# Performance work log

Measured on AMD Instinct MI355X. Metric: run time of the kernel, lower is better.

Reference implementation:

```python
import jax, jax.numpy as jnp
import numpy as np

N_NODES = 8192
IN_F = 16384
OUT_F = 10
N_EDGES = 262144


def setup_inputs() -> dict:
    key = jax.random.key(0)
    ks = jax.random.split(key, 12)
    s = 0.02
    return {
        "x": jax.random.normal(ks[0], (N_NODES, IN_F), dtype=jnp.float32),
        "edge_index": jax.random.randint(ks[1], (2, N_EDGES), 0, N_NODES, dtype=jnp.int64),
        # lin1: in -> 4096, lin2: 4096 -> 2048 (torch Linear: y = x W^T + b)
        "lin1_w": jax.random.normal(ks[2], (4096, IN_F), dtype=jnp.float32) * s,
        "lin1_b": jnp.zeros((4096,), dtype=jnp.float32),
        "lin2_w": jax.random.normal(ks[3], (2048, 4096), dtype=jnp.float32) * s,
        "lin2_b": jnp.zeros((2048,), dtype=jnp.float32),
        # SAGEConv 1: 2048 -> 1024. lin_l (neighbor agg, with bias), lin_r (root, no bias)
        "s1_l_w": jax.random.normal(ks[4], (1024, 2048), dtype=jnp.float32) * s,
        "s1_l_b": jnp.zeros((1024,), dtype=jnp.float32),
        "s1_r_w": jax.random.normal(ks[5], (1024, 2048), dtype=jnp.float32) * s,
        # SAGEConv 2: 1024 -> OUT_F
        "s2_l_w": jax.random.normal(ks[6], (OUT_F, 1024), dtype=jnp.float32) * s,
        "s2_l_b": jnp.zeros((OUT_F,), dtype=jnp.float32),
        "s2_r_w": jax.random.normal(ks[7], (OUT_F, 1024), dtype=jnp.float32) * s,
    }


def reference(x, edge_index, lin1_w, lin1_b, lin2_w, lin2_b,
              s1_l_w, s1_l_b, s1_r_w, s2_l_w, s2_l_b, s2_r_w):
    n = x.shape[0]
    src, dst = edge_index[0], edge_index[1]
    # in-degree for mean aggregation; isolated nodes -> 0 aggregate (PyG behavior)
    deg = jax.ops.segment_sum(jnp.ones_like(dst, dtype=x.dtype), dst, num_segments=n)
    inv_deg = jnp.where(deg > 0, 1.0 / jnp.maximum(deg, 1.0), 0.0)[:, None]

    def sage(h, lw, lb, rw):
        # mean over incoming neighbor messages h[src] scattered to dst
        agg = jax.ops.segment_sum(h[src], dst, num_segments=n) * inv_deg
        return agg @ lw.T + lb + h @ rw.T

    h = jax.nn.relu(x @ lin1_w.T + lin1_b)
    h = jax.nn.relu(h @ lin2_w.T + lin2_b)
    # dropout layers act as identity in eval mode
    h = jax.nn.relu(sage(h, s1_l_w, s1_l_b, s1_r_w))
    h = jax.nn.relu(sage(h, s2_l_w, s2_l_b, s2_r_w))
    return jax.nn.softmax(h, axis=1)
```

## Files before the change

kernel.cpp:

```cpp
#include <hip/hip_runtime.h>


typedef short  short8   __attribute__((ext_vector_type(8)));
typedef float  floatx4  __attribute__((ext_vector_type(4)));
typedef unsigned short ushort8v __attribute__((ext_vector_type(8)));
typedef unsigned short ushort4v __attribute__((ext_vector_type(4)));
typedef unsigned short ushort;

__device__ __forceinline__ ushort f2bf(float f) {
  unsigned u = __float_as_uint(f);
  u += 0x7fffu + ((u >> 16) & 1u);
  return (ushort)(u >> 16);
}
__device__ __forceinline__ float bf2f(ushort h) {
  return __uint_as_float(((unsigned)h) << 16);
}

__device__ __forceinline__ void gload16(const void* g, void* l) {
  __builtin_amdgcn_global_load_lds(
      (const __attribute__((address_space(1))) void*)g,
      (__attribute__((address_space(3))) void*)l, 16, 0, 0);
}

__global__ __launch_bounds__(256) void cvt_f32_bf16(
    const float* __restrict__ in, ushort* __restrict__ out, long n8) {
  long i = (long)blockIdx.x * blockDim.x + threadIdx.x;
  const long stride = (long)gridDim.x * blockDim.x;
  for (; i < n8; i += stride) {
    const float4* p = (const float4*)(in + i * 8);
    float4 a = p[0], b = p[1];
    ushort8v o;
    o[0] = f2bf(a.x); o[1] = f2bf(a.y); o[2] = f2bf(a.z); o[3] = f2bf(a.w);
    o[4] = f2bf(b.x); o[5] = f2bf(b.y); o[6] = f2bf(b.z); o[7] = f2bf(b.w);
    *(ushort8v*)(out + i * 8) = o;
  }
}

__global__ void edge_count(const int* __restrict__ dst, int E, int* __restrict__ deg) {
  int e = blockIdx.x * 256 + threadIdx.x;
  if (e < E) atomicAdd(&deg[dst[e]], 1);
}

__global__ __launch_bounds__(256) void scan_k(
    const int* __restrict__ deg, int* __restrict__ offs, float* __restrict__ inv, int n) {
  __shared__ int part[256];
  const int t = threadIdx.x;
  int local[32];
  int s = 0;
  const int base = t * 32;
#pragma unroll
  for (int i = 0; i < 32; ++i) { local[i] = s; s += deg[base + i]; }
  part[t] = s;
  __syncthreads();
  for (int off = 1; off < 256; off <<= 1) {
    int v = (t >= off) ? part[t - off] : 0;
    __syncthreads();
    part[t] += v;
    __syncthreads();
  }
  const int prev = (t == 0) ? 0 : part[t - 1];
  if (t == 255) offs[n] = part[255];
#pragma unroll
  for (int i = 0; i < 32; ++i) {
    const int e = base + i;
    offs[e] = prev + local[i];
    const int d = deg[e];
    inv[e] = (d > 0) ? (1.0f / (float)d) : 0.0f;
  }
}

__global__ void edge_fill(const int* __restrict__ src, const int* __restrict__ dst, int E,
                          const int* __restrict__ offs, int* __restrict__ fill,
                          int* __restrict__ csr) {
  int e = blockIdx.x * 256 + threadIdx.x;
  if (e < E) {
    const int d = dst[e];
    const int p = offs[d] + atomicAdd(&fill[d], 1);
    csr[p] = src[e];
  }
}

template <int OUT_BF16, int RELU, int HAS_BIAS>
__global__ __launch_bounds__(512, 2) void gemm256(
    const ushort* __restrict__ A, const ushort* __restrict__ Bm,
    const float* __restrict__ bias, void* __restrict__ Cout,
    int M, int N, int K) {
  extern __shared__ char smem[];

  const int nbn = N >> 8;
  const int nbm8 = (M >> 8) >> 3;
  const int x = blockIdx.x & 7;
  const int j = blockIdx.x >> 3;
  const int bm = x * nbm8 + j / nbn;
  const int bn = j % nbn;

  const int t = threadIdx.x;
  const int w = t >> 6, lane = t & 63;
  const int wr = w >> 2, wc = w & 3;

  const int cswz = (t & 7) ^ ((t >> 3) & 7);
  const ushort* Ag = A  + (size_t)(bm * 256 + (t >> 3)) * K + cswz * 8;
  const ushort* Bg = Bm + (size_t)(bn * 256 + (t >> 3)) * K + cswz * 8;
  const int stOff = w * 1024;

  const int rA = wr * 128 + (lane & 15);
  const int rB = wc * 64 + (lane & 15);
  const int s0 = (((lane >> 4) ^ (lane & 7)) << 4);

  floatx4 acc[8][4] = {};
  const int NT = K >> 6;
  const int NIT = NT >> 1;

#define STGA(BUF, KT, H)                                                      \
  {                                                                           \
    const int k0_ = (((KT) < NT) ? (KT) : 0) << 6;                            \
    char* la_ = smem + (BUF) * 65536 + stOff;                                 \
    gload16(Ag + (size_t)(((H) * 2) * 64) * K + k0_, la_ + ((H) * 2) * 8192); \
    gload16(Ag + (size_t)(((H) * 2 + 1) * 64) * K + k0_,                      \
            la_ + ((H) * 2 + 1) * 8192);                                      \
  }
#define STGB(BUF, KT, H)                                                      \
  {                                                                           \
    const int k0_ = (((KT) < NT) ? (KT) : 0) << 6;                            \
    char* lb_ = smem + (BUF) * 65536 + 32768 + stOff;                         \
    gload16(Bg + (size_t)(((H) * 2) * 64) * K + k0_, lb_ + ((H) * 2) * 8192); \
    gload16(Bg + (size_t)(((H) * 2 + 1) * 64) * K + k0_,                      \
            lb_ + ((H) * 2 + 1) * 8192);                                      \
  }

#define PH(BUF, Q, READB, DOWAIT, ...)                                        \
  {                                                                           \
    const char* pa_ = smem + (BUF) * 65536 + rA * 128;                        \
    short8 a00 = *(const short8*)(pa_ + (2 * (Q)) * 2048 + s0);               \
    short8 a01 = *(const short8*)(pa_ + (2 * (Q)) * 2048 + (s0 ^ 64));        \
    short8 a10 = *(const short8*)(pa_ + (2 * (Q) + 1) * 2048 + s0);           \
    short8 a11 = *(const short8*)(pa_ + (2 * (Q) + 1) * 2048 + (s0 ^ 64));    \
    if (READB) {                                                              \
      const char* pb_ = smem + (BUF) * 65536 + 32768 + rB * 128;              \
      _Pragma("unroll") for (int ni = 0; ni < 4; ++ni) {                      \
        bfv0[ni] = *(const short8*)(pb_ + ni * 2048 + s0);                    \
        bfv1[ni] = *(const short8*)(pb_ + ni * 2048 + (s0 ^ 64));             \
      }                                                                       \
    }                                                                         \
    __VA_ARGS__;                                                              \
    if (DOWAIT) asm volatile("s_waitcnt vmcnt(4)" ::: "memory");              \
    __builtin_amdgcn_s_barrier();                                             \
    __builtin_amdgcn_s_setprio(1);                                            \
    _Pragma("unroll") for (int ni = 0; ni < 4; ++ni) {                        \
      acc[2 * (Q)][ni] = __builtin_amdgcn_mfma_f32_16x16x32_bf16(             \
          a00, bfv0[ni], acc[2 * (Q)][ni], 0, 0, 0);                          \
      acc[2 * (Q) + 1][ni] = __builtin_amdgcn_mfma_f32_16x16x32_bf16(         \
          a10, bfv0[ni], acc[2 * (Q) + 1][ni], 0, 0, 0);                      \
    }                                                                         \
    _Pragma("unroll") for (int ni = 0; ni < 4; ++ni) {                        \
      acc[2 * (Q)][ni] = __builtin_amdgcn_mfma_f32_16x16x32_bf16(             \
          a01, bfv1[ni], acc[2 * (Q)][ni], 0, 0, 0);                          \
      acc[2 * (Q) + 1][ni] = __builtin_amdgcn_mfma_f32_16x16x32_bf16(         \
          a11, bfv1[ni], acc[2 * (Q) + 1][ni], 0, 0, 0);                      \
    }                                                                         \
    __builtin_amdgcn_s_setprio(0);                                            \
    asm volatile("" ::: "memory");                                            \
  }

  STGA(0, 0, 0); STGA(0, 0, 1);
  STGB(0, 0, 0); STGB(0, 0, 1);
  STGB(1, 1, 0); STGB(1, 1, 1);
  asm volatile("s_waitcnt vmcnt(4)" ::: "memory");
  __builtin_amdgcn_s_barrier();
  asm volatile("" ::: "memory");

  for (int it = 0; it < NIT; ++it) {
    const int t1 = 2 * it + 1, t2 = 2 * it + 2, t3 = 2 * it + 3;
    short8 bfv0[4], bfv1[4];
    PH(0, 0, 1, 0, STGA(1, t1, 0); STGA(1, t1, 1));
    PH(0, 1, 0, 0, STGB(0, t2, 0));
    PH(0, 2, 0, 0, STGB(0, t2, 1));
    PH(0, 3, 0, 1, );
    PH(1, 0, 1, 0, STGA(0, t2, 0));
    PH(1, 1, 0, 0, STGA(0, t2, 1));
    PH(1, 2, 0, 0, STGB(1, t3, 0));
    PH(1, 3, 0, 1, STGB(1, t3, 1));
  }
  asm volatile("s_waitcnt vmcnt(0)" ::: "memory");

#undef STGA
#undef STGB
#undef PH

  const int row0 = bm * 256 + wr * 128 + ((lane >> 4) << 2);
  const int col0 = bn * 256 + wc * 64 + (lane & 15);
#pragma unroll
  for (int ni = 0; ni < 4; ++ni) {
    const int col = col0 + ni * 16;
    const float bv = HAS_BIAS ? bias[col] : 0.0f;
#pragma unroll
    for (int mi = 0; mi < 8; ++mi) {
#pragma unroll
      for (int j2 = 0; j2 < 4; ++j2) {
        const int row = row0 + mi * 16 + j2;
        float v = acc[mi][ni][j2] + bv;
        if (RELU) v = fmaxf(v, 0.0f);
        if (OUT_BF16)
          ((ushort*)Cout)[(size_t)row * N + col] = f2bf(v);
        else
          ((float*)Cout)[(size_t)row * N + col] = v;
      }
    }
  }
}

__global__ __launch_bounds__(256) void sage1_agg(
    const ushort* __restrict__ hlr1, const int* __restrict__ offs,
    const int* __restrict__ csr, const float* __restrict__ inv,
    const float* __restrict__ lb, ushort* __restrict__ h3) {
  const int dn = blockIdx.x;
  const int f4 = threadIdx.x * 4;
  float ax = 0.f, ay = 0.f, az = 0.f, aw = 0.f;
  const int e0 = offs[dn], e1 = offs[dn + 1];
  for (int e = e0; e < e1; ++e) {
    const int s = csr[e];
    const ushort4v v = *(const ushort4v*)(hlr1 + (size_t)s * 2048 + f4);
    ax += bf2f(v[0]); ay += bf2f(v[1]); az += bf2f(v[2]); aw += bf2f(v[3]);
  }
  const float iv = inv[dn];
  const ushort4v hr = *(const ushort4v*)(hlr1 + (size_t)dn * 2048 + 1024 + f4);
  const float4 bb = *(const float4*)(lb + f4);
  ushort4v o;
  o[0] = f2bf(fmaxf(ax * iv + bb.x + bf2f(hr[0]), 0.0f));
  o[1] = f2bf(fmaxf(ay * iv + bb.y + bf2f(hr[1]), 0.0f));
  o[2] = f2bf(fmaxf(az * iv + bb.z + bf2f(hr[2]), 0.0f));
  o[3] = f2bf(fmaxf(aw * iv + bb.w + bf2f(hr[3]), 0.0f));
  *(ushort4v*)(h3 + (size_t)dn * 1024 + f4) = o;
}

__global__ __launch_bounds__(256) void sage2_mm(
    const ushort* __restrict__ h3, const float* __restrict__ wl,
    const float* __restrict__ wr, float* __restrict__ hl2, float* __restrict__ hr2) {
  __shared__ float wds[20480];
  const int t = threadIdx.x;
  for (int i = t; i < 2560; i += 256)
    *(float4*)&wds[i * 4] = *(const float4*)&wl[i * 4];
  for (int i = t; i < 2560; i += 256)
    *(float4*)&wds[10240 + i * 4] = *(const float4*)&wr[i * 4];
  __syncthreads();

  const int r = t >> 4, c = t & 15;
  const int row = blockIdx.x * 16 + r;

  float hv[64];
#pragma unroll
  for (int ii = 0; ii < 8; ++ii) {
    ushort8v p = *(const ushort8v*)(h3 + (size_t)row * 1024 + c * 64 + ii * 8);
#pragma unroll
    for (int k = 0; k < 8; ++k) hv[ii * 8 + k] = bf2f(p[k]);
  }

  float al[10] = {}, ar[10] = {};
#pragma unroll
  for (int j = 0; j < 10; ++j) {
    const int base = j * 1024 + c * 64;
#pragma unroll
    for (int ii = 0; ii < 16; ++ii) {
      const int f = (ii + c) & 15;
      const float4 lv = *(const float4*)&wds[base + f * 4];
      const float4 rv = *(const float4*)&wds[10240 + base + f * 4];
      const float h0 = hv[f * 4], h1 = hv[f * 4 + 1],
                  h2 = hv[f * 4 + 2], h3v = hv[f * 4 + 3];
      al[j] = fmaf(h0, lv.x, fmaf(h1, lv.y, fmaf(h2, lv.z, fmaf(h3v, lv.w, al[j]))));
      ar[j] = fmaf(h0, rv.x, fmaf(h1, rv.y, fmaf(h2, rv.z, fmaf(h3v, rv.w, ar[j]))));
    }
  }
#pragma unroll
  for (int j = 0; j < 10; ++j) {
#pragma unroll
    for (int off = 8; off > 0; off >>= 1) {
      al[j] += __shfl_down(al[j], off);
      ar[j] += __shfl_down(ar[j], off);
    }
  }
  if (c == 0) {
#pragma unroll
    for (int j = 0; j < 10; ++j) {
      hl2[(size_t)row * 10 + j] = al[j];
      hr2[(size_t)row * 10 + j] = ar[j];
    }
  }
}

__global__ __launch_bounds__(64) void sage2_final(
    const float* __restrict__ hl2, const float* __restrict__ hr2,
    const int* __restrict__ offs, const int* __restrict__ csr,
    const float* __restrict__ inv, const float* __restrict__ lb,
    float* __restrict__ out) {
  const int dn = blockIdx.x;
  const int l = threadIdx.x;
  float a[10] = {};
  const int e0 = offs[dn], e1 = offs[dn + 1];
  for (int e = e0 + l; e < e1; e += 64) {
    const int s = csr[e];
#pragma unroll
    for (int j = 0; j < 10; ++j) a[j] += hl2[(size_t)s * 10 + j];
  }
#pragma unroll
  for (int j = 0; j < 10; ++j)
#pragma unroll
    for (int off = 32; off > 0; off >>= 1) a[j] += __shfl_down(a[j], off);
  if (l == 0) {
    const float iv = inv[dn];
    float v[10];
    float m = -1e30f;
#pragma unroll
    for (int j = 0; j < 10; ++j) {
      v[j] = fmaxf(a[j] * iv + lb[j] + hr2[(size_t)dn * 10 + j], 0.0f);
      m = fmaxf(m, v[j]);
    }
    float ssum = 0.0f;
#pragma unroll
    for (int j = 0; j < 10; ++j) { v[j] = __expf(v[j] - m); ssum += v[j]; }
    const float r = 1.0f / ssum;
#pragma unroll
    for (int j = 0; j < 10; ++j) out[(size_t)dn * 10 + j] = v[j] * r;
  }
}

extern "C" void kernel_launch(void* const* d_in, const int* in_sizes, int n_in,
                              void* d_out, int out_size, void* d_ws, size_t ws_size,
                              hipStream_t stream) {
  const float* x    = (const float*)d_in[0];
  const int*   ei   = (const int*)d_in[1];
  const float* w1   = (const float*)d_in[2];
  const float* b1   = (const float*)d_in[3];
  const float* w2   = (const float*)d_in[4];
  const float* b2   = (const float*)d_in[5];
  const float* s1lw = (const float*)d_in[6];
  const float* s1lb = (const float*)d_in[7];
  const float* s1rw = (const float*)d_in[8];
  const float* s2lw = (const float*)d_in[9];
  const float* s2lb = (const float*)d_in[10];
  const float* s2rw = (const float*)d_in[11];
  float* out = (float*)d_out;
  char* ws = (char*)d_ws;

  const int E = in_sizes[1] / 2;
  const int Nn = 8192;

  hipFuncSetAttribute((const void*)&gemm256<1, 1, 1>,
                      hipFuncAttributeMaxDynamicSharedMemorySize, 131072);
  hipFuncSetAttribute((const void*)&gemm256<1, 0, 0>,
                      hipFuncAttributeMaxDynamicSharedMemorySize, 131072);

  ushort* xb  = (ushort*)(ws + 0L);
  ushort* w1b = (ushort*)(ws + 268435456L);
  ushort* h1  = (ushort*)(ws + 402653184L);
  ushort* w2b = (ushort*)(ws + 469762048L);
  ushort* h2  = (ushort*)(ws + 486539264L);
  ushort* ws1 = (ushort*)(ws + 520093696L);
  char* csrb = ws + 528482304L;
  int*   deg  = (int*)(csrb);
  int*   fill = (int*)(csrb + 32768);
  int*   offs = (int*)(csrb + 65536);
  float* inv  = (float*)(csrb + 98816);
  int*   csr  = (int*)(csrb + 131584);
  ushort* hlr1 = (ushort*)(ws + 0L);
  ushort* h3   = (ushort*)(ws + 67108864L);
  float*  hl2  = (float*)(ws + 83886080L);
  float*  hr2  = (float*)(ws + 84213760L);

  const int* esrc = ei;
  const int* edst = ei + E;

  hipMemsetAsync(deg, 0, 65536, stream);

  cvt_f32_bf16<<<4096, 256, 0, stream>>>(x, xb, 16777216L);
  cvt_f32_bf16<<<2048, 256, 0, stream>>>(w1, w1b, 8388608L);
  cvt_f32_bf16<<<1024, 256, 0, stream>>>(w2, w2b, 1048576L);
  cvt_f32_bf16<<<256, 256, 0, stream>>>(s1lw, ws1, 262144L);
  cvt_f32_bf16<<<256, 256, 0, stream>>>(s1rw, ws1 + 2097152L, 262144L);

  edge_count<<<(E + 255) / 256, 256, 0, stream>>>(edst, E, deg);
  scan_k<<<1, 256, 0, stream>>>(deg, offs, inv, Nn);
  edge_fill<<<(E + 255) / 256, 256, 0, stream>>>(esrc, edst, E, offs, fill, csr);

  gemm256<1, 1, 1><<<512, 512, 131072, stream>>>(xb, w1b, b1, h1, 8192, 4096, 16384);
  gemm256<1, 1, 1><<<256, 512, 131072, stream>>>(h1, w2b, b2, h2, 8192, 2048, 4096);
  gemm256<1, 0, 0><<<256, 512, 131072, stream>>>(h2, ws1, nullptr, hlr1, 8192, 2048, 2048);

  sage1_agg<<<8192, 256, 0, stream>>>(hlr1, offs, csr, inv, s1lb, h3);
  sage2_mm<<<512, 256, 0, stream>>>(h3, s2lw, s2rw, hl2, hr2);
  sage2_final<<<8192, 64, 0, stream>>>(hl2, hr2, offs, csr, inv, s2lb, out);
}
```

Before: 1.365 ms.

## Fuse conversion launches, remap GEMM block swizzle, pack sage2_final nodes per block

Five separate fp32-to-bf16 conversion launches are merged into one grid-stride kernel to cut launch overhead and tail idle time. The GEMM block-index mapping now splits the N dimension, rather than M, across the 8-way XCD grouping, which changes which tiles share L2 on each die. sage2_final now handles four nodes per 256-thread block instead of one node per 64-thread block. The swizzle change assumes N/256 is divisible by 8 and alters cache reuse patterns, which could help or hurt.

```diff
diff --git a/kernel.cpp b/kernel.cpp
--- a/kernel.cpp
+++ b/kernel.cpp
@@ -22,11 +22,10 @@
       (__attribute__((address_space(3))) void*)l, 16, 0, 0);
 }
 
-__global__ __launch_bounds__(256) void cvt_f32_bf16(
-    const float* __restrict__ in, ushort* __restrict__ out, long n8) {
-  long i = (long)blockIdx.x * blockDim.x + threadIdx.x;
-  const long stride = (long)gridDim.x * blockDim.x;
-  for (; i < n8; i += stride) {
+__device__ __forceinline__ void cvt_seg(const float* __restrict__ in,
+                                        ushort* __restrict__ out, long n8,
+                                        long tid, long stride) {
+  for (long i = tid; i < n8; i += stride) {
     const float4* p = (const float4*)(in + i * 8);
     float4 a = p[0], b = p[1];
     ushort8v o;
@@ -34,6 +33,21 @@
     o[4] = f2bf(b.x); o[5] = f2bf(b.y); o[6] = f2bf(b.z); o[7] = f2bf(b.w);
     *(ushort8v*)(out + i * 8) = o;
   }
+}
+
+__global__ __launch_bounds__(256) void cvt_multi(
+    const float* s0, ushort* d0, long n0,
+    const float* s1, ushort* d1, long n1,
+    const float* s2, ushort* d2, long n2,
+    const float* s3, ushort* d3, long n3,
+    const float* s4, ushort* d4, long n4) {
+  const long tid = (long)blockIdx.x * blockDim.x + threadIdx.x;
+  const long stride = (long)gridDim.x * blockDim.x;
+  cvt_seg(s0, d0, n0, tid, stride);
+  cvt_seg(s1, d1, n1, tid, stride);
+  cvt_seg(s2, d2, n2, tid, stride);
+  cvt_seg(s3, d3, n3, tid, stride);
+  cvt_seg(s4, d4, n4, tid, stride);
 }
 
 __global__ void edge_count(const int* __restrict__ dst, int E, int* __restrict__ deg) {
@@ -88,11 +102,11 @@
   extern __shared__ char smem[];
 
   const int nbn = N >> 8;
-  const int nbm8 = (M >> 8) >> 3;
+  const int nbn8 = nbn >> 3;
   const int x = blockIdx.x & 7;
   const int j = blockIdx.x >> 3;
-  const int bm = x * nbm8 + j / nbn;
-  const int bn = j % nbn;
+  const int bn = x * nbn8 + j % nbn8;
+  const int bm = j / nbn8;
 
   const int t = threadIdx.x;
   const int w = t >> 6, lane = t & 63;
@@ -287,13 +301,13 @@
   }
 }
 
-__global__ __launch_bounds__(64) void sage2_final(
+__global__ __launch_bounds__(256) void sage2_final(
     const float* __restrict__ hl2, const float* __restrict__ hr2,
     const int* __restrict__ offs, const int* __restrict__ csr,
     const float* __restrict__ inv, const float* __restrict__ lb,
     float* __restrict__ out) {
-  const int dn = blockIdx.x;
-  const int l = threadIdx.x;
+  const int dn = blockIdx.x * 4 + (threadIdx.x >> 6);
+  const int l = threadIdx.x & 63;
   float a[10] = {};
   const int e0 = offs[dn], e1 = offs[dn + 1];
   for (int e = e0 + l; e < e1; e += 64) {
@@ -371,11 +385,12 @@
 
   hipMemsetAsync(deg, 0, 65536, stream);
 
-  cvt_f32_bf16<<<4096, 256, 0, stream>>>(x, xb, 16777216L);
-  cvt_f32_bf16<<<2048, 256, 0, stream>>>(w1, w1b, 8388608L);
-  cvt_f32_bf16<<<1024, 256, 0, stream>>>(w2, w2b, 1048576L);
-  cvt_f32_bf16<<<256, 256, 0, stream>>>(s1lw, ws1, 262144L);
-  cvt_f32_bf16<<<256, 256, 0, stream>>>(s1rw, ws1 + 2097152L, 262144L);
+  cvt_multi<<<4096, 256, 0, stream>>>(
+      x, xb, 16777216L,
+      w1, w1b, 8388608L,
+      w2, w2b, 1048576L,
+      s1lw, ws1, 262144L,
+      s1rw, ws1 + 2097152L, 262144L);
 
   edge_count<<<(E + 255) / 256, 256, 0, stream>>>(edst, E, deg);
   scan_k<<<1, 256, 0, stream>>>(deg, offs, inv, Nn);
@@ -387,5 +402,5 @@
 
   sage1_agg<<<8192, 256, 0, stream>>>(hlr1, offs, csr, inv, s1lb, h3);
   sage2_mm<<<512, 256, 0, stream>>>(h3, s2lw, s2rw, hl2, hr2);
-  sage2_final<<<8192, 64, 0, stream>>>(hl2, hr2, offs, csr, inv, s2lb, out);
-}
+  sage2_final<<<2048, 256, 0, stream>>>(hl2, hr2, offs, csr, inv, s2lb, out);
+}
```

Result: slower. 1.407 ms (+3.1%).
